# Optimization experiments

Hardware: AMD Instinct MI355X
Metric: run time of the kernel (lower is better)

The kernel has to match this reference:

```python
import jax, jax.numpy as jnp
import numpy as np

B, S, D, H = 2, 2048, 1024, 16
HD = D // H  # 64
MASK_VAL = -10000.0


def setup_inputs() -> dict:
    key = jax.random.key(0)
    ks = jax.random.split(key, 8)
    sc = 0.02
    q_features = jax.random.normal(ks[0], (B, S, D), jnp.float32)
    kv_features = jax.random.normal(ks[1], (B, S, D), jnp.float32)
    # causal mask, broadcastable (1,1,S,S)
    mask = jnp.tril(jnp.ones((S, S), jnp.bool_))[None, None]
    Wq = jax.random.normal(ks[2], (D, D), jnp.float32) * sc
    bq = jnp.zeros((D,), jnp.float32)
    Wkv = jax.random.normal(ks[3], (D, 2 * D), jnp.float32) * sc
    bkv = jnp.zeros((2 * D,), jnp.float32)
    Wp = jax.random.normal(ks[4], (D, D), jnp.float32) * sc
    bp = jnp.zeros((D,), jnp.float32)
    return {"q_features": q_features, "kv_features": kv_features, "mask": mask,
            "Wq": Wq, "bq": bq, "Wkv": Wkv, "bkv": bkv, "Wp": Wp, "bp": bp}


def _split_heads(t):
    # (B,S,D) -> (B,H,S,HD)
    return t.reshape(B, S, H, HD).transpose(0, 2, 1, 3)


def reference(q_features, kv_features, mask, Wq, bq, Wkv, bkv, Wp, bp):
    query = q_features @ Wq + bq            # (B,S,D)
    kv = kv_features @ Wkv + bkv            # (B,S,2D)
    key, value = jnp.split(kv, 2, axis=-1)
    q = _split_heads(query)                 # (B,H,S,HD)
    k = _split_heads(key)
    v = _split_heads(value)
    scores = jnp.einsum('bhqd,bhkd->bhqk', q, k) / jnp.sqrt(jnp.float32(HD))
    scores = jnp.where(mask, scores, jnp.asarray(MASK_VAL, scores.dtype))
    attn = jax.nn.softmax(scores, axis=-1)  # (B,H,S,S)
    out = jnp.einsum('bhqk,bhkd->bhqd', attn, v)
    out = out.transpose(0, 2, 1, 3).reshape(B, S, D)  # merge heads
    return out @ Wp + bp
```

## Files before the change

### kernel.cpp

```cpp
#include <hip/hip_runtime.h>

typedef unsigned short u16;
typedef unsigned int u32;
typedef __attribute__((ext_vector_type(4))) unsigned short us4;
typedef __attribute__((ext_vector_type(8))) unsigned short us8;
typedef __attribute__((ext_vector_type(4))) short s16x4;
typedef __attribute__((ext_vector_type(8))) __bf16 bf16x8;
typedef __attribute__((ext_vector_type(4))) float floatx4;

#define S_ 2048
#define D_ 1024
#define QSC 0.18033688f

__device__ __forceinline__ float b2f(u16 u) {
  unsigned v = ((unsigned)u) << 16;
  return __builtin_bit_cast(float, v);
}
__device__ __forceinline__ u16 f2bf(float f) {
  unsigned u = __builtin_bit_cast(unsigned, f);
  unsigned r = (u + 0x7fffu + ((u >> 16) & 1u)) >> 16;
  return (u16)r;
}
__device__ __forceinline__ u16 f2bf_rhu(float f) {
  return (u16)((__builtin_bit_cast(unsigned, f) + 0x8000u) >> 16);
}

typedef const __attribute__((address_space(1))) u32* gas_t;
typedef __attribute__((address_space(3))) u32* las_t;
__device__ __forceinline__ void gload16(const u16* g, u16* l) {
  __builtin_amdgcn_global_load_lds((gas_t)g, (las_t)l, 16, 0, 0);
}

#define PBAR()                                   \
  {                                              \
    __builtin_amdgcn_sched_barrier(0);           \
    asm volatile("" ::: "memory");               \
    __builtin_amdgcn_s_barrier();                \
    asm volatile("" ::: "memory");               \
    __builtin_amdgcn_sched_barrier(0);           \
  }
#define WAITVM(N) asm volatile("s_waitcnt vmcnt(" #N ")" ::: "memory")

__global__ __launch_bounds__(256) void prep(
    const float* __restrict__ qf, const float* __restrict__ kvf,
    const float* __restrict__ Wq, const float* __restrict__ Wkv,
    const float* __restrict__ Wp, u16* __restrict__ qa, u16* __restrict__ kva,
    u16* __restrict__ Wqt, u16* __restrict__ Wkvt, u16* __restrict__ Wpt) {
  int bid = blockIdx.x, tid = threadIdx.x;
  if (bid < 4096) {
    const float* src = (bid < 2048) ? qf : kvf;
    u16* dst = (bid < 2048) ? qa : kva;
    size_t i = ((size_t)(bid & 2047) * 256 + tid) * 8;
    floatx4 a = *(const floatx4*)(src + i);
    floatx4 b = *(const floatx4*)(src + i + 4);
    us8 r;
#pragma unroll
    for (int j = 0; j < 4; j++) { r[j] = f2bf(a[j]); r[4 + j] = f2bf(b[j]); }
    *(us8*)(dst + i) = r;
  } else {
    int t = bid - 4096;
    const float* src; u16* dst; int R, C;
    if (t < 1024)      { src = Wq;  dst = Wqt;  R = 1024; C = 1024; }
    else if (t < 3072) { t -= 1024; src = Wkv; dst = Wkvt; R = 1024; C = 2048; }
    else               { t -= 3072; src = Wp;  dst = Wpt;  R = 1024; C = 1024; }
    int bx = t % (C >> 5), by = t / (C >> 5);
    __shared__ u16 tile[32][33];
    int tx = tid & 31, ty = tid >> 5;
    int x = bx * 32 + tx;
    for (int i = ty; i < 32; i += 8)
      tile[i][tx] = f2bf(src[(size_t)(by * 32 + i) * C + x]);
    __syncthreads();
    int ox = by * 32 + tx;
    for (int i = ty; i < 32; i += 8)
      dst[(size_t)(bx * 32 + i) * R + ox] = tile[tx][i];
  }
}

template <int MODE>
__device__ __forceinline__ void gemm256(
    const u16* __restrict__ A, const u16* __restrict__ Bt,
    const float* __restrict__ bias, void* __restrict__ C0,
    u16* __restrict__ C1, int N, int m0, int n0, u16* smem, float cscale) {
  int tid = threadIdx.x;
  int w = tid >> 6, lane = tid & 63;
  int quad = lane >> 4, l16 = lane & 15;
  int wr = w >> 2, wc = w & 3;

  int srow = w * 32 + (lane >> 2);
  int gchunk = ((lane & 3) ^ ((lane >> 3) & 3)) << 3;
  const u16* Asrc = A + (size_t)(m0 + srow) * 1024 + gchunk;
  const u16* Bsrc = Bt + (size_t)(n0 + srow) * 1024 + gchunk;
  u16* Adst = smem + w * 1024;
  u16* Bdst = smem + 32768 + w * 1024;

  int swz = (quad ^ ((l16 >> 1) & 3)) << 3;
  int aoff = (wr * 128 + l16) * 32 + swz;
  int boff = 32768 + (wc * 64 + l16) * 32 + swz;

  floatx4 acc[8][4] = {};

#define STAGE_A(t)                                             \
  {                                                            \
    int s_ = (t) & 3;                                          \
    gload16(Asrc + (t) * 32, Adst + s_ * 8192);                \
    gload16(Asrc + (t) * 32 + 16384, Adst + s_ * 8192 + 512);  \
  }
#define STAGE_B(t)                                             \
  {                                                            \
    int s_ = (t) & 3;                                          \
    gload16(Bsrc + (t) * 32, Bdst + s_ * 8192);                \
    gload16(Bsrc + (t) * 32 + 16384, Bdst + s_ * 8192 + 512);  \
  }

  STAGE_A(0); STAGE_B(0); STAGE_A(1); STAGE_B(1); STAGE_A(2); STAGE_B(2);
  WAITVM(8);
  PBAR();

  bf16x8 af[4], bf[4];

#define PHASE_A(t, DOSTAGE)                                                 \
  {                                                                         \
    int s_ = (t) & 3;                                                       \
    _Pragma("unroll") for (int mf = 0; mf < 4; mf++)                        \
        af[mf] = __builtin_bit_cast(                                        \
            bf16x8, *(const us8*)&smem[s_ * 8192 + aoff + mf * 512]);       \
    _Pragma("unroll") for (int nf = 0; nf < 4; nf++)                        \
        bf[nf] = __builtin_bit_cast(                                        \
            bf16x8, *(const us8*)&smem[s_ * 8192 + boff + nf * 512]);       \
    if (DOSTAGE) STAGE_A((t) + 3);                                          \
    PBAR();                                                                 \
    __builtin_amdgcn_s_setprio(1);                                          \
    _Pragma("unroll") for (int mf = 0; mf < 4; mf++)                        \
        _Pragma("unroll") for (int nf = 0; nf < 4; nf++)                    \
            acc[mf][nf] = __builtin_amdgcn_mfma_f32_16x16x32_bf16(          \
                af[mf], bf[nf], acc[mf][nf], 0, 0, 0);                      \
    __builtin_amdgcn_s_setprio(0);                                          \
    PBAR();                                                                 \
  }
#define PHASE_B(t, DOSTAGE, VMW)                                            \
  {                                                                         \
    int s_ = (t) & 3;                                                       \
    _Pragma("unroll") for (int mf = 0; mf < 4; mf++)                        \
        af[mf] = __builtin_bit_cast(                                        \
            bf16x8,                                                         \
            *(const us8*)&smem[s_ * 8192 + aoff + 2048 + mf * 512]);        \
    if (DOSTAGE) STAGE_B((t) + 3);                                          \
    PBAR();                                                                 \
    __builtin_amdgcn_s_setprio(1);                                          \
    _Pragma("unroll") for (int mf = 0; mf < 4; mf++)                        \
        _Pragma("unroll") for (int nf = 0; nf < 4; nf++)                    \
            acc[4 + mf][nf] = __builtin_amdgcn_mfma_f32_16x16x32_bf16(      \
                af[mf], bf[nf], acc[4 + mf][nf], 0, 0, 0);                  \
    __builtin_amdgcn_s_setprio(0);                                          \
    VMW;                                                                    \
    PBAR();                                                                 \
  }

#pragma unroll 1
  for (int t = 0; t < 29; t++) {
    PHASE_A(t, true);
    PHASE_B(t, true, WAITVM(4));
  }
  PHASE_A(29, false); PHASE_B(29, false, (void)0);
  PHASE_A(30, false); PHASE_B(30, false, WAITVM(0));
  PHASE_A(31, false); PHASE_B(31, false, (void)0);

#undef PHASE_A
#undef PHASE_B
#undef STAGE_A
#undef STAGE_B

#pragma unroll
  for (int mf = 0; mf < 8; mf++) {
#pragma unroll
    for (int nf = 0; nf < 4; nf++) {
      int col = n0 + wc * 64 + nf * 16 + l16;
      int rowq = m0 + wr * 128 + mf * 16 + quad * 4;
      float bv = bias[col];
      if (MODE == 0) {
        u16* o = (u16*)C0;
#pragma unroll
        for (int r = 0; r < 4; r++)
          o[(size_t)(rowq + r) * N + col] = f2bf((acc[mf][nf][r] + bv) * cscale);
      } else {
        if (col < 1024) {
          u16* o = (u16*)C0;
#pragma unroll
          for (int r = 0; r < 4; r++)
            o[(size_t)(rowq + r) * 1024 + col] = f2bf(acc[mf][nf][r] + bv);
        } else {
          int vcol = col - 1024;
          int b = rowq >> 11, s0 = rowq & 2047;
          us4 pv;
#pragma unroll
          for (int r = 0; r < 4; r++) pv[r] = f2bf(acc[mf][nf][r] + bv);
          *(us4*)&C1[((size_t)(b * 1024 + vcol)) * (size_t)S_ + s0] = pv;
        }
      }
    }
  }
}

__global__ __launch_bounds__(512, 2) void gemm_qkv(
    const u16* __restrict__ qa, const u16* __restrict__ kva,
    const u16* __restrict__ Wqt, const u16* __restrict__ Wkvt,
    const float* __restrict__ bq, const float* __restrict__ bkv,
    u16* __restrict__ Qb, u16* __restrict__ Kb, u16* __restrict__ Vt) {
  __shared__ __align__(16) u16 smem[65536];
  int bid = blockIdx.x;
  if (bid < 64) {
    gemm256<0>(qa, Wqt, bq, Qb, nullptr, 1024,
               (bid >> 2) * 256, (bid & 3) * 256, smem, QSC);
  } else {
    int lb = bid - 64;
    gemm256<2>(kva, Wkvt, bkv, Kb, Vt, 2048,
               (lb >> 3) * 256, (lb & 7) * 256, smem, 1.0f);
  }
}

template <int TM, int TN, int MODE>
__device__ __forceinline__ void gemm_core(
    const u16* __restrict__ A, const u16* __restrict__ Bt,
    const float* __restrict__ bias, void* __restrict__ C0,
    u16* __restrict__ C1, int N, int n0, int m0,
    u16* As, u16* Bs, float cscale) {
  constexpr int MT = TM / 32, NT = TN / 32;
  int tid  = threadIdx.x;
  int wave = tid >> 6, lane = tid & 63;
  int quad = lane >> 4, l16 = lane & 15;
  int wr = wave >> 1, wc = wave & 1;
  const u16* Ag = A  + (size_t)(m0 + wave * 8 + (lane >> 3)) * 1024 + (lane & 7) * 8;
  const u16* Bg = Bt + (size_t)(n0 + wave * 8 + (lane >> 3)) * 1024 + (lane & 7) * 8;
  u16* Aw = As + wave * 8 * 64;
  u16* Bw = Bs + wave * 8 * 64;
  floatx4 acc[MT][NT] = {};
  for (int k0 = 0; k0 < 1024; k0 += 64) {
    if (k0) __syncthreads();
#pragma unroll
    for (int p = 0; p < TM / 32; p++)
      gload16(Ag + (size_t)p * 32 * 1024 + k0, Aw + p * 32 * 64);
#pragma unroll
    for (int p = 0; p < TN / 32; p++)
      gload16(Bg + (size_t)p * 32 * 1024 + k0, Bw + p * 32 * 64);
    __syncthreads();
#pragma unroll
    for (int kk = 0; kk < 2; kk++) {
      bf16x8 af[MT], bf[NT];
#pragma unroll
      for (int mt = 0; mt < MT; mt++)
        af[mt] = __builtin_bit_cast(bf16x8,
            *(const us8*)&As[(wr * (TM / 2) + mt * 16 + l16) * 64 + (kk * 4 + quad) * 8]);
#pragma unroll
      for (int nt = 0; nt < NT; nt++)
        bf[nt] = __builtin_bit_cast(bf16x8,
            *(const us8*)&Bs[(wc * (TN / 2) + nt * 16 + l16) * 64 + (kk * 4 + quad) * 8]);
#pragma unroll
      for (int mt = 0; mt < MT; mt++)
#pragma unroll
        for (int nt = 0; nt < NT; nt++)
          acc[mt][nt] = __builtin_amdgcn_mfma_f32_16x16x32_bf16(
              af[mt], bf[nt], acc[mt][nt], 0, 0, 0);
    }
  }
#pragma unroll
  for (int mt = 0; mt < MT; mt++) {
#pragma unroll
    for (int nt = 0; nt < NT; nt++) {
      int col  = n0 + wc * (TN / 2) + nt * 16 + l16;
      int rowq = m0 + wr * (TM / 2) + mt * 16 + quad * 4;
      float bv = bias[col];
      if (MODE == 0) {
        u16* o = (u16*)C0;
#pragma unroll
        for (int r = 0; r < 4; r++)
          o[(size_t)(rowq + r) * N + col] = f2bf((acc[mt][nt][r] + bv) * cscale);
      } else if (MODE == 1) {
        float* o = (float*)C0;
#pragma unroll
        for (int r = 0; r < 4; r++)
          o[(size_t)(rowq + r) * N + col] = acc[mt][nt][r] + bv;
      } else {
        if (col < 1024) {
          u16* o = (u16*)C0;
#pragma unroll
          for (int r = 0; r < 4; r++)
            o[(size_t)(rowq + r) * 1024 + col] = f2bf(acc[mt][nt][r] + bv);
        } else {
          int vcol = col - 1024;
          int b = rowq >> 11, s0 = rowq & 2047;
          us4 pv;
#pragma unroll
          for (int r = 0; r < 4; r++) pv[r] = f2bf(acc[mt][nt][r] + bv);
          *(us4*)&C1[((size_t)(b * 1024 + vcol)) * (size_t)S_ + s0] = pv;
        }
      }
    }
  }
}

__global__ __launch_bounds__(256) void gemm_out(
    const u16* __restrict__ AO, const u16* __restrict__ Wpt,
    const float* __restrict__ bp, float* __restrict__ out) {
  __shared__ __align__(16) u16 As[64 * 64];
  __shared__ __align__(16) u16 Bs[128 * 64];
  gemm_core<64, 128, 1>(AO, Wpt, bp, out, nullptr, 1024,
                        (blockIdx.x & 7) * 128, (blockIdx.x >> 3) * 64, As, Bs, 1.0f);
}

__global__ __launch_bounds__(256) void attn_fwd(
    const u16* __restrict__ Q, const u16* __restrict__ Kb,
    const u16* __restrict__ Vt, u16* __restrict__ O,
    u16* __restrict__ Opart, float* __restrict__ ml) {
  __shared__ __align__(16) u16 Ks[64 * 64];
  __shared__ __align__(16) u16 Vs[64 * 64];
  int tid  = threadIdx.x;
  int wave = tid >> 6, lane = tid & 63;
  int quad = lane >> 4, l16 = lane & 15;
  int bh = blockIdx.x, b = bh >> 4, h = bh & 15;
  int y = blockIdx.y;
  int qt, kb0, kb1, half = 0;
  bool split = (y < 32);
  if (split) {
    qt = 31 - (y >> 1);
    half = y & 1;
    int h1 = (qt + 1) >> 1;
    kb0 = half ? h1 : 0;
    kb1 = half ? (qt + 1) : h1;
  } else {
    qt = 47 - y;
    kb0 = 0; kb1 = qt + 1;
  }
  const size_t row0 = (size_t)b * S_;
  const u16* Kg = Kb + row0 * D_ + h * 64;
  const u16* Vg = Vt + ((size_t)b * 1024 + h * 64) * S_;

  int qrow = qt * 64 + wave * 16 + l16;
  const u16* qp = Q + (row0 + qrow) * D_ + h * 64 + quad * 8;
  bf16x8 aqv[2];
  aqv[0] = __builtin_bit_cast(bf16x8, *(const us8*)(qp));
  aqv[1] = __builtin_bit_cast(bf16x8, *(const us8*)(qp + 32));

  floatx4 o_[4] = {};
  floatx4 l_acc = {};
  const s16x4 ones4 = {0x3F80, 0x3F80, 0x3F80, 0x3F80};

  int lr = lane >> 3, c8 = lane & 7;
  int r0 = wave * 16 + lr;
  int r1 = r0 + 8;
  us8 pk0 = *(const us8*)(Kg + (size_t)(kb0 * 64 + r0) * D_ + c8 * 8);
  us8 pk1 = *(const us8*)(Kg + (size_t)(kb0 * 64 + r1) * D_ + c8 * 8);
  us8 pv0 = *(const us8*)(Vg + (size_t)r0 * S_ + kb0 * 64 + c8 * 8);
  us8 pv1 = *(const us8*)(Vg + (size_t)r1 * S_ + kb0 * 64 + c8 * 8);

  for (int kb = kb0; kb < kb1; kb++) {
    __syncthreads();
    *(us8*)&Ks[r0 * 64 + ((c8 ^ (r0 & 7)) << 3)] = pk0;
    *(us8*)&Ks[r1 * 64 + ((c8 ^ (r1 & 7)) << 3)] = pk1;
    *(us8*)&Vs[r0 * 64 + ((c8 ^ (r0 & 7)) << 3)] = pv0;
    *(us8*)&Vs[r1 * 64 + ((c8 ^ (r1 & 7)) << 3)] = pv1;
    if (kb + 1 < kb1) {
      int koff = (kb + 1) * 64;
      pk0 = *(const us8*)(Kg + (size_t)(koff + r0) * D_ + c8 * 8);
      pk1 = *(const us8*)(Kg + (size_t)(koff + r1) * D_ + c8 * 8);
      pv0 = *(const us8*)(Vg + (size_t)r0 * S_ + koff + c8 * 8);
      pv1 = *(const us8*)(Vg + (size_t)r1 * S_ + koff + c8 * 8);
    }
    __syncthreads();

    floatx4 s[4] = {};
#pragma unroll
    for (int kk = 0; kk < 2; kk++)
#pragma unroll
      for (int nt = 0; nt < 4; nt++) {
        us8 kf = *(const us8*)&Ks[(nt * 16 + l16) * 64 +
                                  (((kk * 4 + quad) ^ (l16 & 7)) << 3)];
        s[nt] = __builtin_amdgcn_mfma_f32_16x16x32_bf16(
            __builtin_bit_cast(bf16x8, kf), aqv[kk], s[nt], 0, 0, 0);
      }

    if (kb == qt) {
      int qg = wave * 16 + l16;
#pragma unroll
      for (int nt = 0; nt < 4; nt++)
#pragma unroll
        for (int r = 0; r < 4; r++)
          if (nt * 16 + quad * 4 + r > qg) s[nt][r] = -1e5f;
    }

    s16x4 pb[4];
#pragma unroll
    for (int nt = 0; nt < 4; nt++)
#pragma unroll
      for (int r = 0; r < 4; r++)
        pb[nt][r] = (short)f2bf_rhu(__builtin_amdgcn_exp2f(s[nt][r]));

#pragma unroll
    for (int nt = 0; nt < 4; nt++) {
      l_acc = __builtin_amdgcn_mfma_f32_16x16x16bf16_1k(ones4, pb[nt], l_acc, 0, 0, 0);
#pragma unroll
      for (int mt = 0; mt < 4; mt++) {
        int hd = mt * 16 + l16;
        int chunk = nt * 2 + (quad >> 1);
        us4 vf = *(const us4*)&Vs[hd * 64 + ((chunk ^ (l16 & 7)) << 3) + (quad & 1) * 4];
        o_[mt] = __builtin_amdgcn_mfma_f32_16x16x16bf16_1k(
            __builtin_bit_cast(s16x4, vf), pb[nt], o_[mt], 0, 0, 0);
      }
    }
  }

  if (!split) {
    float rl = __builtin_amdgcn_rcpf(l_acc[0]);
    size_t orow = (row0 + qt * 64 + wave * 16 + l16) * D_ + h * 64;
#pragma unroll
    for (int mt = 0; mt < 4; mt++) {
      us4 ov;
#pragma unroll
      for (int r = 0; r < 4; r++) ov[r] = f2bf(o_[mt][r] * rl);
      *(us4*)&O[orow + mt * 16 + quad * 4] = ov;
    }
  } else {
    int pb_ = (qt - 16) * 2 + half;
    u16* op = Opart + ((size_t)(bh * 32 + pb_)) * 4096;
    int qrow_l = wave * 16 + l16;
#pragma unroll
    for (int mt = 0; mt < 4; mt++) {
      us4 ov;
#pragma unroll
      for (int r = 0; r < 4; r++) ov[r] = f2bf(o_[mt][r]);
      *(us4*)&op[qrow_l * 64 + mt * 16 + quad * 4] = ov;
    }
    if (quad == 0)
      ml[(size_t)(bh * 32 + pb_) * 64 + qrow_l] = l_acc[0];
  }
}

__global__ __launch_bounds__(256) void combine(
    const u16* __restrict__ Opart, const float* __restrict__ ml,
    u16* __restrict__ O) {
  int bh = blockIdx.x, b = bh >> 4, h = bh & 15;
  int qt = 16 + blockIdx.y;
  int base = bh * 32 + (qt - 16) * 2;
  const u16* o1 = Opart + (size_t)base * 4096;
  const u16* o2 = o1 + 4096;
  int row = threadIdx.x >> 2, cg = (threadIdx.x & 3) * 16;
  float l1 = ml[(size_t)base * 64 + row];
  float l2 = ml[(size_t)(base + 1) * 64 + row];
  float inv = __builtin_amdgcn_rcpf(l1 + l2);
  size_t orow = ((size_t)b * S_ + qt * 64 + row) * D_ + h * 64 + cg;
#pragma unroll
  for (int v = 0; v < 2; v++) {
    us8 x1 = *(const us8*)&o1[row * 64 + cg + v * 8];
    us8 x2 = *(const us8*)&o2[row * 64 + cg + v * 8];
    us8 out;
#pragma unroll
    for (int j = 0; j < 8; j++)
      out[j] = f2bf((b2f(x1[j]) + b2f(x2[j])) * inv);
    *(us8*)&O[orow + v * 8] = out;
  }
}

extern "C" void kernel_launch(void* const* d_in, const int* in_sizes, int n_in,
                              void* d_out, int out_size, void* d_ws, size_t ws_size,
                              hipStream_t stream) {
  const float* qf  = (const float*)d_in[0];
  const float* kvf = (const float*)d_in[1];
  const float* Wq  = (const float*)d_in[3];
  const float* bq  = (const float*)d_in[4];
  const float* Wkv = (const float*)d_in[5];
  const float* bkv = (const float*)d_in[6];
  const float* Wp  = (const float*)d_in[7];
  const float* bp  = (const float*)d_in[8];

  char* ws = (char*)d_ws;
  const size_t MB = 1048576;
  u16*   kva  = (u16*)(ws);
  u16*   AO   = (u16*)(ws);
  u16*   Kbp  = (u16*)(ws + 8 * MB);
  u16*   Vtp  = (u16*)(ws + 16 * MB);
  u16*   Wqt  = (u16*)(ws + 24 * MB);
  float* mlp  = (float*)(ws + 24 * MB);
  u16*   Wkvt = (u16*)(ws + 26 * MB);
  u16*   Wpt  = (u16*)(ws + 30 * MB);
  u16*   qa    = (u16*)d_out;
  u16*   Opart = (u16*)d_out;
  u16*   Qb    = (u16*)d_out + (size_t)4 * 1048576;

  prep<<<8192, 256, 0, stream>>>(qf, kvf, Wq, Wkv, Wp, qa, kva, Wqt, Wkvt, Wpt);
  gemm_qkv<<<192, 512, 0, stream>>>(qa, kva, Wqt, Wkvt, bq, bkv, Qb, Kbp, Vtp);
  attn_fwd<<<dim3(32, 48), 256, 0, stream>>>(Qb, Kbp, Vtp, AO, Opart, mlp);
  combine<<<dim3(32, 16), 256, 0, stream>>>(Opart, mlp, AO);
  gemm_out<<<512, 256, 0, stream>>>(AO, Wpt, bp, (float*)d_out);
}
```

Baseline: 217.4 us.

## Use 128-row query tiles with 8 waves and double-buffered K/V in attention

The attention kernel now processes 128 query rows per block with 512 threads, so each K/V tile loaded into shared memory is reused by twice as many query rows. K/V staging is double-buffered, with a single barrier per iteration, and MFMA sections are wrapped in s_setprio. The split/combine scheme and its block schedule table are remapped to the larger tiles. In exchange there are fewer blocks (768 instead of 1536) and some waves idle on the diagonal tiles, where kb > dkb is skipped.

```diff
diff --git a/kernel.cpp b/kernel.cpp
--- a/kernel.cpp
+++ b/kernel.cpp
@@ -307,35 +307,37 @@
                         (blockIdx.x & 7) * 128, (blockIdx.x >> 3) * 64, As, Bs, 1.0f);
 }
 
-__global__ __launch_bounds__(256) void attn_fwd(
+__global__ __launch_bounds__(512) void attn_fwd(
     const u16* __restrict__ Q, const u16* __restrict__ Kb,
     const u16* __restrict__ Vt, u16* __restrict__ O,
     u16* __restrict__ Opart, float* __restrict__ ml) {
-  __shared__ __align__(16) u16 Ks[64 * 64];
-  __shared__ __align__(16) u16 Vs[64 * 64];
+  __shared__ __align__(16) u16 sm[16384];
   int tid  = threadIdx.x;
-  int wave = tid >> 6, lane = tid & 63;
+  int w    = tid >> 6, lane = tid & 63;
   int quad = lane >> 4, l16 = lane & 15;
   int bh = blockIdx.x, b = bh >> 4, h = bh & 15;
   int y = blockIdx.y;
-  int qt, kb0, kb1, half = 0;
-  bool split = (y < 32);
-  if (split) {
-    qt = 31 - (y >> 1);
-    half = y & 1;
-    int h1 = (qt + 1) >> 1;
-    kb0 = half ? h1 : 0;
-    kb1 = half ? (qt + 1) : h1;
-  } else {
-    qt = 47 - y;
-    kb0 = 0; kb1 = qt + 1;
-  }
+
+  static const signed char yt_[24] = {15,15,7,14,14,13,13,6,12,12,11,11,5,
+                                      10,10,9,9,4,8,8,3,2,1,0};
+  static const signed char yh_[24] = {0,1,-1,0,1,0,1,-1,0,1,0,1,-1,
+                                      0,1,0,1,-1,0,1,-1,-1,-1,-1};
+  int t = yt_[y], hh = yh_[y];
+  bool split = hh >= 0;
+  int kb0, kb1;
+  if (split) { kb0 = hh ? (t + 1) : 0; kb1 = hh ? (2 * t + 2) : (t + 1); }
+  else       { kb0 = 0; kb1 = 2 * t + 2; }
+  int n = kb1 - kb0;
+
   const size_t row0 = (size_t)b * S_;
   const u16* Kg = Kb + row0 * D_ + h * 64;
   const u16* Vg = Vt + ((size_t)b * 1024 + h * 64) * S_;
 
-  int qrow = qt * 64 + wave * 16 + l16;
-  const u16* qp = Q + (row0 + qrow) * D_ + h * 64 + quad * 8;
+  int qlo = t * 128 + w * 16;
+  int dkb = qlo >> 6;
+  int qg  = (qlo & 63) + l16;
+
+  const u16* qp = Q + (row0 + qlo + l16) * D_ + h * 64 + quad * 8;
   bf16x8 aqv[2];
   aqv[0] = __builtin_bit_cast(bf16x8, *(const us8*)(qp));
   aqv[1] = __builtin_bit_cast(bf16x8, *(const us8*)(qp + 32));
@@ -344,73 +346,87 @@
   floatx4 l_acc = {};
   const s16x4 ones4 = {0x3F80, 0x3F80, 0x3F80, 0x3F80};
 
-  int lr = lane >> 3, c8 = lane & 7;
-  int r0 = wave * 16 + lr;
-  int r1 = r0 + 8;
-  us8 pk0 = *(const us8*)(Kg + (size_t)(kb0 * 64 + r0) * D_ + c8 * 8);
-  us8 pk1 = *(const us8*)(Kg + (size_t)(kb0 * 64 + r1) * D_ + c8 * 8);
-  us8 pv0 = *(const us8*)(Vg + (size_t)r0 * S_ + kb0 * 64 + c8 * 8);
-  us8 pv1 = *(const us8*)(Vg + (size_t)r1 * S_ + kb0 * 64 + c8 * 8);
-
-  for (int kb = kb0; kb < kb1; kb++) {
+  int srow = tid >> 3, c8 = tid & 7;
+  int woff = srow * 64 + ((c8 ^ (srow & 7)) << 3);
+  u16* smK = sm;
+  u16* smV = sm + 8192;
+
+  const u16* Kp = Kg + (size_t)(kb0 * 64 + srow) * D_ + c8 * 8;
+  const u16* Vp = Vg + (size_t)srow * S_ + kb0 * 64 + c8 * 8;
+  us8 pk = *(const us8*)Kp, pv = *(const us8*)Vp;
+  *(us8*)&smK[woff] = pk;
+  *(us8*)&smV[woff] = pv;
+  if (n > 1) {
+    Kp += (size_t)64 * D_; Vp += 64;
+    pk = *(const us8*)Kp; pv = *(const us8*)Vp;
+  }
+  __syncthreads();
+
+  for (int i = 0; i < n; i++) {
+    int cur = i & 1;
+    int kb = kb0 + i;
+    if (i + 1 < n) {
+      int nxt = (cur ^ 1) * 4096;
+      *(us8*)&smK[nxt + woff] = pk;
+      *(us8*)&smV[nxt + woff] = pv;
+      if (i + 2 < n) {
+        Kp += (size_t)64 * D_; Vp += 64;
+        pk = *(const us8*)Kp; pv = *(const us8*)Vp;
+      }
+    }
+    if (kb <= dkb) {
+      const u16* Ksb = smK + cur * 4096;
+      const u16* Vsb = smV + cur * 4096;
+
+      floatx4 s[4] = {};
+      __builtin_amdgcn_s_setprio(1);
+#pragma unroll
+      for (int kk = 0; kk < 2; kk++)
+#pragma unroll
+        for (int nt = 0; nt < 4; nt++) {
+          us8 kf = *(const us8*)&Ksb[(nt * 16 + l16) * 64 +
+                                     (((kk * 4 + quad) ^ (l16 & 7)) << 3)];
+          s[nt] = __builtin_amdgcn_mfma_f32_16x16x32_bf16(
+              __builtin_bit_cast(bf16x8, kf), aqv[kk], s[nt], 0, 0, 0);
+        }
+      __builtin_amdgcn_s_setprio(0);
+
+      if (kb == dkb) {
+#pragma unroll
+        for (int nt = 0; nt < 4; nt++)
+#pragma unroll
+          for (int r = 0; r < 4; r++)
+            if (nt * 16 + quad * 4 + r > qg) s[nt][r] = -1e5f;
+      }
+
+      s16x4 pb[4];
+#pragma unroll
+      for (int nt = 0; nt < 4; nt++)
+#pragma unroll
+        for (int r = 0; r < 4; r++)
+          pb[nt][r] = (short)f2bf_rhu(__builtin_amdgcn_exp2f(s[nt][r]));
+
+      __builtin_amdgcn_s_setprio(1);
+#pragma unroll
+      for (int nt = 0; nt < 4; nt++) {
+        l_acc = __builtin_amdgcn_mfma_f32_16x16x16bf16_1k(ones4, pb[nt], l_acc, 0, 0, 0);
+#pragma unroll
+        for (int mt = 0; mt < 4; mt++) {
+          int hd = mt * 16 + l16;
+          int chunk = nt * 2 + (quad >> 1);
+          us4 vf = *(const us4*)&Vsb[hd * 64 + ((chunk ^ (l16 & 7)) << 3) + (quad & 1) * 4];
+          o_[mt] = __builtin_amdgcn_mfma_f32_16x16x16bf16_1k(
+              __builtin_bit_cast(s16x4, vf), pb[nt], o_[mt], 0, 0, 0);
+        }
+      }
+      __builtin_amdgcn_s_setprio(0);
+    }
     __syncthreads();
-    *(us8*)&Ks[r0 * 64 + ((c8 ^ (r0 & 7)) << 3)] = pk0;
-    *(us8*)&Ks[r1 * 64 + ((c8 ^ (r1 & 7)) << 3)] = pk1;
-    *(us8*)&Vs[r0 * 64 + ((c8 ^ (r0 & 7)) << 3)] = pv0;
-    *(us8*)&Vs[r1 * 64 + ((c8 ^ (r1 & 7)) << 3)] = pv1;
-    if (kb + 1 < kb1) {
-      int koff = (kb + 1) * 64;
-      pk0 = *(const us8*)(Kg + (size_t)(koff + r0) * D_ + c8 * 8);
-      pk1 = *(const us8*)(Kg + (size_t)(koff + r1) * D_ + c8 * 8);
-      pv0 = *(const us8*)(Vg + (size_t)r0 * S_ + koff + c8 * 8);
-      pv1 = *(const us8*)(Vg + (size_t)r1 * S_ + koff + c8 * 8);
-    }
-    __syncthreads();
-
-    floatx4 s[4] = {};
-#pragma unroll
-    for (int kk = 0; kk < 2; kk++)
-#pragma unroll
-      for (int nt = 0; nt < 4; nt++) {
-        us8 kf = *(const us8*)&Ks[(nt * 16 + l16) * 64 +
-                                  (((kk * 4 + quad) ^ (l16 & 7)) << 3)];
-        s[nt] = __builtin_amdgcn_mfma_f32_16x16x32_bf16(
-            __builtin_bit_cast(bf16x8, kf), aqv[kk], s[nt], 0, 0, 0);
-      }
-
-    if (kb == qt) {
-      int qg = wave * 16 + l16;
-#pragma unroll
-      for (int nt = 0; nt < 4; nt++)
-#pragma unroll
-        for (int r = 0; r < 4; r++)
-          if (nt * 16 + quad * 4 + r > qg) s[nt][r] = -1e5f;
-    }
-
-    s16x4 pb[4];
-#pragma unroll
-    for (int nt = 0; nt < 4; nt++)
-#pragma unroll
-      for (int r = 0; r < 4; r++)
-        pb[nt][r] = (short)f2bf_rhu(__builtin_amdgcn_exp2f(s[nt][r]));
-
-#pragma unroll
-    for (int nt = 0; nt < 4; nt++) {
-      l_acc = __builtin_amdgcn_mfma_f32_16x16x16bf16_1k(ones4, pb[nt], l_acc, 0, 0, 0);
-#pragma unroll
-      for (int mt = 0; mt < 4; mt++) {
-        int hd = mt * 16 + l16;
-        int chunk = nt * 2 + (quad >> 1);
-        us4 vf = *(const us4*)&Vs[hd * 64 + ((chunk ^ (l16 & 7)) << 3) + (quad & 1) * 4];
-        o_[mt] = __builtin_amdgcn_mfma_f32_16x16x16bf16_1k(
-            __builtin_bit_cast(s16x4, vf), pb[nt], o_[mt], 0, 0, 0);
-      }
-    }
   }
 
   if (!split) {
     float rl = __builtin_amdgcn_rcpf(l_acc[0]);
-    size_t orow = (row0 + qt * 64 + wave * 16 + l16) * D_ + h * 64;
+    size_t orow = (row0 + qlo + l16) * D_ + h * 64;
 #pragma unroll
     for (int mt = 0; mt < 4; mt++) {
       us4 ov;
@@ -419,18 +435,18 @@
       *(us4*)&O[orow + mt * 16 + quad * 4] = ov;
     }
   } else {
-    int pb_ = (qt - 16) * 2 + half;
-    u16* op = Opart + ((size_t)(bh * 32 + pb_)) * 4096;
-    int qrow_l = wave * 16 + l16;
+    int part = (t - 8) * 2 + hh;
+    u16* op = Opart + ((size_t)(bh * 16 + part)) * 8192;
+    int rloc = w * 16 + l16;
 #pragma unroll
     for (int mt = 0; mt < 4; mt++) {
       us4 ov;
 #pragma unroll
       for (int r = 0; r < 4; r++) ov[r] = f2bf(o_[mt][r]);
-      *(us4*)&op[qrow_l * 64 + mt * 16 + quad * 4] = ov;
+      *(us4*)&op[rloc * 64 + mt * 16 + quad * 4] = ov;
     }
     if (quad == 0)
-      ml[(size_t)(bh * 32 + pb_) * 64 + qrow_l] = l_acc[0];
+      ml[(size_t)(bh * 16 + part) * 128 + rloc] = l_acc[0];
   }
 }
 
@@ -438,19 +454,19 @@
     const u16* __restrict__ Opart, const float* __restrict__ ml,
     u16* __restrict__ O) {
   int bh = blockIdx.x, b = bh >> 4, h = bh & 15;
-  int qt = 16 + blockIdx.y;
-  int base = bh * 32 + (qt - 16) * 2;
-  const u16* o1 = Opart + (size_t)base * 4096;
-  const u16* o2 = o1 + 4096;
-  int row = threadIdx.x >> 2, cg = (threadIdx.x & 3) * 16;
-  float l1 = ml[(size_t)base * 64 + row];
-  float l2 = ml[(size_t)(base + 1) * 64 + row];
+  int t = 8 + blockIdx.y;
+  int p0 = bh * 16 + (t - 8) * 2;
+  const u16* o1 = Opart + (size_t)p0 * 8192;
+  const u16* o2 = o1 + 8192;
+  int row = threadIdx.x >> 1, ch = (threadIdx.x & 1) * 32;
+  float l1 = ml[(size_t)p0 * 128 + row];
+  float l2 = ml[(size_t)(p0 + 1) * 128 + row];
   float inv = __builtin_amdgcn_rcpf(l1 + l2);
-  size_t orow = ((size_t)b * S_ + qt * 64 + row) * D_ + h * 64 + cg;
-#pragma unroll
-  for (int v = 0; v < 2; v++) {
-    us8 x1 = *(const us8*)&o1[row * 64 + cg + v * 8];
-    us8 x2 = *(const us8*)&o2[row * 64 + cg + v * 8];
+  size_t orow = ((size_t)b * S_ + t * 128 + row) * D_ + h * 64 + ch;
+#pragma unroll
+  for (int v = 0; v < 4; v++) {
+    us8 x1 = *(const us8*)&o1[row * 64 + ch + v * 8];
+    us8 x2 = *(const us8*)&o2[row * 64 + ch + v * 8];
     us8 out;
 #pragma unroll
     for (int j = 0; j < 8; j++)
@@ -487,7 +503,7 @@
 
   prep<<<8192, 256, 0, stream>>>(qf, kvf, Wq, Wkv, Wp, qa, kva, Wqt, Wkvt, Wpt);
   gemm_qkv<<<192, 512, 0, stream>>>(qa, kva, Wqt, Wkvt, bq, bkv, Qb, Kbp, Vtp);
-  attn_fwd<<<dim3(32, 48), 256, 0, stream>>>(Qb, Kbp, Vtp, AO, Opart, mlp);
-  combine<<<dim3(32, 16), 256, 0, stream>>>(Opart, mlp, AO);
+  attn_fwd<<<dim3(32, 24), 512, 0, stream>>>(Qb, Kbp, Vtp, AO, Opart, mlp);
+  combine<<<dim3(32, 8), 256, 0, stream>>>(Opart, mlp, AO);
   gemm_out<<<512, 256, 0, stream>>>(AO, Wpt, bp, (float*)d_out);
 }
```

Result: no change. 214.8 us (-1.2%).
